# Kernel tuning notes

Measured on AMD Instinct MI355X. Metric: run time of the kernel, lower is better.

Reference implementation:

```python
import jax, jax.numpy as jnp
import numpy as np

N_NODES = 50000
N_EDGES = 800000
D_FEAT = 128
UNITS = 256
K = 3


def setup_inputs() -> dict:
    key = jax.random.key(0)
    k1, k2, k3, k4 = jax.random.split(key, 4)
    x = jax.random.normal(k1, (N_NODES, D_FEAT), dtype=jnp.float32)
    edge_index = jax.random.randint(k2, (2, N_EDGES), 0, N_NODES, dtype=jnp.int32)
    edge_weight = jnp.ones((N_EDGES,), dtype=jnp.float32)
    # glorot-uniform kernel [(K+1)*D, UNITS], zero bias
    fan_in, fan_out = D_FEAT * (K + 1), UNITS
    limit = np.sqrt(6.0 / (fan_in + fan_out)).astype(np.float32)
    kernel = jax.random.uniform(k3, (fan_in, fan_out), minval=-limit, maxval=limit, dtype=jnp.float32)
    bias = jnp.zeros((UNITS,), dtype=jnp.float32)
    return {"x": x, "edge_index": edge_index, "edge_weight": edge_weight,
            "kernel": kernel, "bias": bias}


def reference(x, edge_index, edge_weight, kernel, bias):
    n = x.shape[0]
    row, col = edge_index[0], edge_index[1]
    # symmetric GCN normalization (renorm=False: normalize first, then self-loops w=1)
    deg = jax.ops.segment_sum(edge_weight, row, num_segments=n)
    deg_inv_sqrt = jnp.where(deg > 0, jax.lax.rsqrt(jnp.where(deg > 0, deg, 1.0)), 0.0)
    normed_w = deg_inv_sqrt[row] * edge_weight * deg_inv_sqrt[col]
    loop = jnp.arange(n, dtype=row.dtype)
    row2 = jnp.concatenate([row, loop])
    col2 = jnp.concatenate([col, loop])
    w2 = jnp.concatenate([normed_w, jnp.ones((n,), dtype=normed_w.dtype)])
    # K-hop propagation, collecting each hop
    xs = [x]
    h = x
    for _ in range(K):
        msg = h[col2] * w2[:, None]            # [E+N, D] gather + scale
        h = jax.ops.segment_sum(msg, row2, num_segments=n)  # scatter-sum
        xs.append(h)
    hcat = jnp.concatenate(xs, axis=-1)        # [N, (K+1)*D]
    out = hcat @ kernel + bias
    return jax.nn.relu(out)
```

## Files before the change

### kernel.cpp

```cpp
#include <hip/hip_runtime.h>

#define NN 50000
#define NP 50048
#define NE 800000
#define D 128
#define UNITS 256
#define KTOT 512
#define SCAN_NB 50
#define NREP 16
#define CONV_NB 6250

typedef __attribute__((ext_vector_type(8))) short short8;
typedef __attribute__((ext_vector_type(4))) float floatx4;

__device__ inline unsigned short f2b(float f) {
    unsigned u = __float_as_uint(f);
    return (unsigned short)((u + 0x7fff + ((u >> 16) & 1)) >> 16);
}
__device__ inline float2 bx2f(unsigned v) {
    float2 r;
    r.x = __uint_as_float(v << 16);
    r.y = __uint_as_float(v & 0xffff0000u);
    return r;
}

__global__ void count_kernel(const int* __restrict__ row, int* __restrict__ cnt16,
                             int* __restrict__ rank, int E) {
    int e = blockIdx.x * blockDim.x + threadIdx.x;
    if (e < E) {
        int rep = (e >> 6) & (NREP - 1);
        rank[e] = atomicAdd(&cnt16[rep * NN + row[e]], 1);
    }
}

__global__ __launch_bounds__(256) void scanA_kernel(int* __restrict__ cnt16,
                                                    int* __restrict__ row_ptr,
                                                    int* __restrict__ bsum) {
    __shared__ int s[256];
    int b = blockIdx.x, t = threadIdx.x;
    int base = b * 1024 + t * 4;
    int v[4];
    int sum = 0;
#pragma unroll
    for (int i = 0; i < 4; ++i) {
        int idx = base + i;
        int tot = 0;
        if (idx < NN) {
            int c[NREP];
            int run = 0;
#pragma unroll
            for (int r = 0; r < NREP; ++r) c[r] = cnt16[r * NN + idx];
#pragma unroll
            for (int r = 0; r < NREP; ++r) {
                cnt16[r * NN + idx] = run;
                run += c[r];
            }
            tot = run;
        }
        v[i] = tot;
        sum += tot;
    }
    s[t] = sum;
    __syncthreads();
    for (int off = 1; off < 256; off <<= 1) {
        int add = (t >= off) ? s[t - off] : 0;
        __syncthreads();
        s[t] += add;
        __syncthreads();
    }
    int run = s[t] - sum;
#pragma unroll
    for (int i = 0; i < 4; ++i) {
        int idx = base + i;
        if (idx < NN) row_ptr[idx] = run;
        run += v[i];
    }
    if (t == 255) bsum[b] = s[255];
}

__global__ void scanB_kernel(int* __restrict__ bsum, int* __restrict__ row_ptr) {
    if (threadIdx.x == 0 && blockIdx.x == 0) {
        int run = 0;
        for (int i = 0; i < SCAN_NB; ++i) {
            int v = bsum[i];
            bsum[i] = run;
            run += v;
        }
        row_ptr[NN] = run;
    }
}

__global__ __launch_bounds__(256) void scanC_kernel(int* __restrict__ row_ptr,
                                                    const int* __restrict__ bsum) {
    int b = blockIdx.x, t = threadIdx.x;
    int off = bsum[b];
    int base = b * 1024 + t * 4;
#pragma unroll
    for (int i = 0; i < 4; ++i) {
        int idx = base + i;
        if (idx < NN) row_ptr[idx] += off;
    }
}

__global__ void fill_kernel(const int* __restrict__ row, const int* __restrict__ col,
                            const float* __restrict__ w, const int* __restrict__ rank,
                            const int* __restrict__ row_ptr, const int* __restrict__ cnt16,
                            int2* __restrict__ edges, int E) {
    int e = blockIdx.x * blockDim.x + threadIdx.x;
    if (e >= E) return;
    int r = row[e];
    int rep = (e >> 6) & (NREP - 1);
    int pos = row_ptr[r] + cnt16[rep * NN + r] + rank[e];
    edges[pos] = make_int2(col[e], __float_as_int(w[e]));
}

__global__ __launch_bounds__(256) void degdis_kernel(const int* __restrict__ row_ptr,
                                                     const int2* __restrict__ edges,
                                                     float* __restrict__ dis) {
    int node = blockIdx.x * 4 + (threadIdx.x >> 6);
    int l = threadIdx.x & 63;
    if (node >= NN) return;
    int beg = row_ptr[node], end = row_ptr[node + 1];
    float s = 0.f;
    for (int e = beg + l; e < end; e += 64) s += __int_as_float(edges[e].y);
#pragma unroll
    for (int off = 32; off; off >>= 1) s += __shfl_down(s, off);
    if (l == 0) dis[node] = s > 0.f ? rsqrtf(s) : 0.f;
}

__global__ __launch_bounds__(256) void prep_kernel(const float* __restrict__ x,
                                                   unsigned* __restrict__ xb,
                                                   const float* __restrict__ W,
                                                   short* __restrict__ Wt) {
    __shared__ float tile[32][33];
    if (blockIdx.x < CONV_NB) {
        int t = blockIdx.x * 256 + threadIdx.x;
        float4 v = ((const float4*)x)[t];
        uint2 o;
        o.x = (unsigned)f2b(v.x) | ((unsigned)f2b(v.y) << 16);
        o.y = (unsigned)f2b(v.z) | ((unsigned)f2b(v.w) << 16);
        ((uint2*)xb)[t] = o;
    } else {
        int b = blockIdx.x - CONV_NB;
        int kb = (b & 15) * 32;
        int nb = (b >> 4) * 32;
        int tx = threadIdx.x & 31, ty = threadIdx.x >> 5;
        for (int i = 0; i < 32; i += 8)
            tile[ty + i][tx] = W[(size_t)(kb + ty + i) * UNITS + nb + tx];
        __syncthreads();
        for (int i = 0; i < 32; i += 8)
            Wt[(size_t)(nb + ty + i) * KTOT + kb + tx] = (short)f2b(tile[tx][ty + i]);
    }
}

__device__ inline void acc8(float* acc, uint4 v, float w) {
    float2 f0 = bx2f(v.x), f1 = bx2f(v.y), f2 = bx2f(v.z), f3 = bx2f(v.w);
    acc[0] = fmaf(w, f0.x, acc[0]); acc[1] = fmaf(w, f0.y, acc[1]);
    acc[2] = fmaf(w, f1.x, acc[2]); acc[3] = fmaf(w, f1.y, acc[3]);
    acc[4] = fmaf(w, f2.x, acc[4]); acc[5] = fmaf(w, f2.y, acc[5]);
    acc[6] = fmaf(w, f3.x, acc[6]); acc[7] = fmaf(w, f3.y, acc[7]);
}

template <bool NORM>
__global__ __launch_bounds__(256) void gather_kernel(const unsigned* __restrict__ hprev,
                                                     unsigned* __restrict__ hnext,
                                                     const int* __restrict__ row_ptr,
                                                     int2* __restrict__ edges,
                                                     const float* __restrict__ dis) {
    int node = blockIdx.x * 4 + (threadIdx.x >> 6);
    if (node >= NN) return;
    int l = threadIdx.x & 63;
    int g = l >> 4;
    int s = l & 15;
    const uint4* hp4 = (const uint4*)hprev;
    int beg = row_ptr[node], end = row_ptr[node + 1];
    float dr = NORM ? dis[node] : 1.f;

    float acc[8] = {0.f, 0.f, 0.f, 0.f, 0.f, 0.f, 0.f, 0.f};
    int2 M0 = edges[(beg + g) < end ? (beg + g) : end - 1];
    int2 M1 = edges[(beg + 4 + g) < end ? (beg + 4 + g) : end - 1];
    for (int e = beg; e < end; e += 8) {
        int i0 = e + g;
        int i1 = e + 4 + g;
        int2 E0 = M0, E1 = M1;
        int en = e + 8;
        if (en < end) {
            int j0 = en + g, j1 = en + 4 + g;
            M0 = edges[j0 < end ? j0 : end - 1];
            M1 = edges[j1 < end ? j1 : end - 1];
        }
        float w0 = __int_as_float(E0.y);
        float w1 = __int_as_float(E1.y);
        if (NORM) {
            w0 *= dr * dis[E0.x];
            w1 *= dr * dis[E1.x];
        }
        w0 = (i0 < end) ? w0 : 0.f;
        w1 = (i1 < end) ? w1 : 0.f;
        uint4 v0 = hp4[(size_t)E0.x * 16 + s];
        uint4 v1 = hp4[(size_t)E1.x * 16 + s];
        acc8(acc, v0, w0);
        acc8(acc, v1, w1);
        if (NORM && s == 0) {
            if (i0 < end) edges[i0].y = __float_as_int(w0);
            if (i1 < end) edges[i1].y = __float_as_int(w1);
        }
    }
#pragma unroll
    for (int i = 0; i < 8; ++i) {
        acc[i] += __shfl_xor(acc[i], 16);
        acc[i] += __shfl_xor(acc[i], 32);
    }
    if (g == 0) {
        uint4 sv = hp4[(size_t)node * 16 + s];
        acc8(acc, sv, 1.f);
        uint4 o;
        o.x = (unsigned)f2b(acc[0]) | ((unsigned)f2b(acc[1]) << 16);
        o.y = (unsigned)f2b(acc[2]) | ((unsigned)f2b(acc[3]) << 16);
        o.z = (unsigned)f2b(acc[4]) | ((unsigned)f2b(acc[5]) << 16);
        o.w = (unsigned)f2b(acc[6]) | ((unsigned)f2b(acc[7]) << 16);
        ((uint4*)hnext)[(size_t)node * 16 + s] = o;
    }
}

#define BK 64
#define GLDS(g, l)                                                                      \
    __builtin_amdgcn_global_load_lds((const __attribute__((address_space(1))) void*)(g), \
                                     (__attribute__((address_space(3))) void*)(l), 16, 0, 0)

__global__ __launch_bounds__(256) void gemm_mfma(const short* __restrict__ A0,
                                                 const short* __restrict__ Wt,
                                                 const float* __restrict__ bias,
                                                 float* __restrict__ C) {
    __shared__ short As[128 * BK];
    __shared__ short Bs[128 * BK];
    const int t = threadIdx.x;
    const int m0 = blockIdx.x * 128;
    const int n0 = blockIdx.y * 128;
    const int w = t >> 6;
    const int l = t & 63;
    const int wr = (w >> 1) * 64;
    const int wc = (w & 1) * 64;
    const int lm = l & 15;
    const int lg = l >> 4;

    const int srow = l >> 3;
    const int soff = ((l & 7) ^ srow) * 8;

    floatx4 zero = {0.f, 0.f, 0.f, 0.f};
    floatx4 acc[4][4];
#pragma unroll
    for (int r = 0; r < 4; ++r)
#pragma unroll
        for (int c = 0; c < 4; ++c) acc[r][c] = zero;

    for (int kk = 0; kk < KTOT; kk += BK) {
        const short* Asrc = A0 + (size_t)(kk >> 7) * ((size_t)NP * 128) + (kk & 127);
        const short* Bsrc = Wt + kk;
#pragma unroll
        for (int i = 0; i < 4; ++i) {
            int seg = w * 4 + i;
            int row = seg * 8 + srow;
            GLDS(Asrc + (size_t)(m0 + row) * D + soff, As + seg * 512);
            GLDS(Bsrc + (size_t)(n0 + row) * KTOT + soff, Bs + seg * 512);
        }
        __syncthreads();
#pragma unroll
        for (int j = 0; j < 2; ++j) {
            short8 af[4], bfr[4];
#pragma unroll
            for (int r = 0; r < 4; ++r) {
                int row = wr + r * 16 + lm;
                int ch = (lg + 4 * j) ^ (row & 7);
                af[r] = *(const short8*)&As[row * BK + ch * 8];
            }
#pragma unroll
            for (int c = 0; c < 4; ++c) {
                int row = wc + c * 16 + lm;
                int ch = (lg + 4 * j) ^ (row & 7);
                bfr[c] = *(const short8*)&Bs[row * BK + ch * 8];
            }
#pragma unroll
            for (int r = 0; r < 4; ++r)
#pragma unroll
                for (int c = 0; c < 4; ++c)
                    acc[r][c] = __builtin_amdgcn_mfma_f32_16x16x32_bf16(af[r], bfr[c],
                                                                        acc[r][c], 0, 0, 0);
        }
        __syncthreads();
    }

    const int q4 = lg * 4;
#pragma unroll
    for (int r = 0; r < 4; ++r) {
#pragma unroll
        for (int i = 0; i < 4; ++i) {
            int m = m0 + wr + r * 16 + q4 + i;
            if (m < NN) {
#pragma unroll
                for (int c = 0; c < 4; ++c) {
                    int n = n0 + wc + c * 16 + lm;
                    float v = acc[r][c][i] + bias[n];
                    C[(size_t)m * UNITS + n] = fmaxf(v, 0.f);
                }
            }
        }
    }
}

extern "C" void kernel_launch(void* const* d_in, const int* in_sizes, int n_in,
                              void* d_out, int out_size, void* d_ws, size_t ws_size,
                              hipStream_t stream) {
    const float* x = (const float*)d_in[0];
    const int* ei = (const int*)d_in[1];
    const float* ew_in = (const float*)d_in[2];
    const float* W = (const float*)d_in[3];
    const float* bias = (const float*)d_in[4];
    float* out = (float*)d_out;

    const int* row = ei;
    const int* col = ei + NE;

    float* dis = (float*)d_ws;
    int* cnt16 = (int*)(dis + NN);
    int* rank = cnt16 + NREP * NN;
    int* bsum = rank + NE;
    int* row_ptr = bsum + 64;
    int2* edges = (int2*)(row_ptr + NN + 2);
    unsigned* xb = (unsigned*)(edges + NE) + 2;
    unsigned* h1b = xb + (size_t)NP * 64;
    unsigned* h2b = h1b + (size_t)NP * 64;
    unsigned* h3b = h2b + (size_t)NP * 64;
    short* Wt = (short*)(h3b + (size_t)NP * 64);

    hipMemsetAsync(cnt16, 0, NREP * NN * sizeof(int), stream);

    count_kernel<<<(NE + 255) / 256, 256, 0, stream>>>(row, cnt16, rank, NE);
    scanA_kernel<<<SCAN_NB, 256, 0, stream>>>(cnt16, row_ptr, bsum);
    scanB_kernel<<<1, 64, 0, stream>>>(bsum, row_ptr);
    scanC_kernel<<<SCAN_NB, 256, 0, stream>>>(row_ptr, bsum);
    fill_kernel<<<(NE + 255) / 256, 256, 0, stream>>>(row, col, ew_in, rank, row_ptr, cnt16,
                                                      edges, NE);
    degdis_kernel<<<(NN + 3) / 4, 256, 0, stream>>>(row_ptr, edges, dis);
    prep_kernel<<<CONV_NB + 128, 256, 0, stream>>>(x, xb, W, Wt);

    int gat_blocks = (NN + 3) / 4;
    gather_kernel<true><<<gat_blocks, 256, 0, stream>>>(xb, h1b, row_ptr, edges, dis);
    gather_kernel<false><<<gat_blocks, 256, 0, stream>>>(h1b, h2b, row_ptr, edges, dis);
    gather_kernel<false><<<gat_blocks, 256, 0, stream>>>(h2b, h3b, row_ptr, edges, dis);

    gemm_mfma<<<dim3(NP / 128, UNITS / 128), 256, 0, stream>>>(
        (const short*)xb, Wt, bias, out);
}
```

Baseline: 315.3 us.

## Fuse preprocessing kernels, compute degree by atomics, widen gather, double-buffer GEMM

The count, x/W conversion and degree computation now run in one launch, with degree accumulated by float atomics instead of a separate CSR-walking kernel. The scan drops its single-thread middle kernel and instead has each block reduce the preceding block sums. The gather loop handles 16 edges per iteration with four outstanding row loads, up from 8. The GEMM moves to 64x128 tiles with BK=32 and double-buffered LDS staging. Together these cut launch count and improve overlap, at the cost of atomic contention on the degree array and more GEMM iterations.

```diff
diff --git a/kernel.cpp b/kernel.cpp
--- a/kernel.cpp
+++ b/kernel.cpp
@@ -6,9 +6,10 @@
 #define D 128
 #define UNITS 256
 #define KTOT 512
-#define SCAN_NB 50
+#define SCAN_NB 196
 #define NREP 16
 #define CONV_NB 6250
+#define COUNT_NB 3125
 
 typedef __attribute__((ext_vector_type(8))) short short8;
 typedef __attribute__((ext_vector_type(4))) float floatx4;
@@ -24,43 +25,69 @@
     return r;
 }
 
-__global__ void count_kernel(const int* __restrict__ row, int* __restrict__ cnt16,
-                             int* __restrict__ rank, int E) {
-    int e = blockIdx.x * blockDim.x + threadIdx.x;
-    if (e < E) {
-        int rep = (e >> 6) & (NREP - 1);
-        rank[e] = atomicAdd(&cnt16[rep * NN + row[e]], 1);
+__global__ __launch_bounds__(256) void count_prep_kernel(const int* __restrict__ row,
+                                                         const float* __restrict__ ew,
+                                                         int* __restrict__ cnt16,
+                                                         float* __restrict__ deg,
+                                                         int* __restrict__ rank,
+                                                         const float* __restrict__ x,
+                                                         unsigned* __restrict__ xb,
+                                                         const float* __restrict__ W,
+                                                         short* __restrict__ Wt) {
+    __shared__ float tile[32][33];
+    int b = blockIdx.x;
+    if (b < COUNT_NB) {
+        int e = b * 256 + threadIdx.x;
+        if (e < NE) {
+            int r = row[e];
+            int rep = (e >> 6) & (NREP - 1);
+            rank[e] = atomicAdd(&cnt16[rep * NN + r], 1);
+            atomicAdd(&deg[r], ew[e]);
+        }
+    } else if (b < COUNT_NB + CONV_NB) {
+        int t = (b - COUNT_NB) * 256 + threadIdx.x;
+        float4 v = ((const float4*)x)[t];
+        uint2 o;
+        o.x = (unsigned)f2b(v.x) | ((unsigned)f2b(v.y) << 16);
+        o.y = (unsigned)f2b(v.z) | ((unsigned)f2b(v.w) << 16);
+        ((uint2*)xb)[t] = o;
+    } else {
+        int bb = b - COUNT_NB - CONV_NB;
+        int kb = (bb & 15) * 32;
+        int nb = (bb >> 4) * 32;
+        int tx = threadIdx.x & 31, ty = threadIdx.x >> 5;
+        for (int i = 0; i < 32; i += 8)
+            tile[ty + i][tx] = W[(size_t)(kb + ty + i) * UNITS + nb + tx];
+        __syncthreads();
+        for (int i = 0; i < 32; i += 8)
+            Wt[(size_t)(nb + ty + i) * KTOT + kb + tx] = (short)f2b(tile[tx][ty + i]);
     }
 }
 
 __global__ __launch_bounds__(256) void scanA_kernel(int* __restrict__ cnt16,
+                                                    const float* __restrict__ deg,
+                                                    float* __restrict__ dis,
                                                     int* __restrict__ row_ptr,
                                                     int* __restrict__ bsum) {
     __shared__ int s[256];
-    int b = blockIdx.x, t = threadIdx.x;
-    int base = b * 1024 + t * 4;
-    int v[4];
-    int sum = 0;
-#pragma unroll
-    for (int i = 0; i < 4; ++i) {
-        int idx = base + i;
-        int tot = 0;
-        if (idx < NN) {
-            int c[NREP];
-            int run = 0;
-#pragma unroll
-            for (int r = 0; r < NREP; ++r) c[r] = cnt16[r * NN + idx];
-#pragma unroll
-            for (int r = 0; r < NREP; ++r) {
-                cnt16[r * NN + idx] = run;
-                run += c[r];
-            }
-            tot = run;
-        }
-        v[i] = tot;
-        sum += tot;
-    }
-    s[t] = sum;
+    int t = threadIdx.x;
+    int idx = blockIdx.x * 256 + t;
+    int tot = 0;
+    if (idx < NN) {
+        int c[NREP];
+#pragma unroll
+        for (int r = 0; r < NREP; ++r) c[r] = cnt16[r * NN + idx];
+        int run = 0;
+#pragma unroll
+        for (int r = 0; r < NREP; ++r) {
+            cnt16[r * NN + idx] = run;
+            run += c[r];
+        }
+        tot = run;
+        float dv = deg[idx];
+        dis[idx] = dv > 0.f ? rsqrtf(dv) : 0.f;
+    }
+    s[t] = tot;
     __syncthreads();
     for (int off = 1; off < 256; off <<= 1) {
         int add = (t >= off) ? s[t - off] : 0;
@@ -68,38 +95,25 @@
         s[t] += add;
         __syncthreads();
     }
-    int run = s[t] - sum;
-#pragma unroll
-    for (int i = 0; i < 4; ++i) {
-        int idx = base + i;
-        if (idx < NN) row_ptr[idx] = run;
-        run += v[i];
-    }
-    if (t == 255) bsum[b] = s[255];
-}
-
-__global__ void scanB_kernel(int* __restrict__ bsum, int* __restrict__ row_ptr) {
-    if (threadIdx.x == 0 && blockIdx.x == 0) {
-        int run = 0;
-        for (int i = 0; i < SCAN_NB; ++i) {
-            int v = bsum[i];
-            bsum[i] = run;
-            run += v;
-        }
-        row_ptr[NN] = run;
-    }
+    if (idx < NN) row_ptr[idx] = s[t] - tot;
+    if (t == 255) bsum[blockIdx.x] = s[255];
 }
 
 __global__ __launch_bounds__(256) void scanC_kernel(int* __restrict__ row_ptr,
                                                     const int* __restrict__ bsum) {
+    __shared__ int soff_s;
     int b = blockIdx.x, t = threadIdx.x;
-    int off = bsum[b];
-    int base = b * 1024 + t * 4;
-#pragma unroll
-    for (int i = 0; i < 4; ++i) {
-        int idx = base + i;
-        if (idx < NN) row_ptr[idx] += off;
-    }
+    if (t < 64) {
+        int acc = 0;
+        for (int i = t; i < b; i += 64) acc += bsum[i];
+#pragma unroll
+        for (int off = 32; off; off >>= 1) acc += __shfl_down(acc, off);
+        if (t == 0) soff_s = acc;
+    }
+    __syncthreads();
+    int idx = b * 256 + t;
+    if (idx < NN) row_ptr[idx] += soff_s;
+    if (b == 0 && t == 0) row_ptr[NN] = NE;
 }
 
 __global__ void fill_kernel(const int* __restrict__ row, const int* __restrict__ col,
@@ -112,45 +126,6 @@
     int rep = (e >> 6) & (NREP - 1);
     int pos = row_ptr[r] + cnt16[rep * NN + r] + rank[e];
     edges[pos] = make_int2(col[e], __float_as_int(w[e]));
-}
-
-__global__ __launch_bounds__(256) void degdis_kernel(const int* __restrict__ row_ptr,
-                                                     const int2* __restrict__ edges,
-                                                     float* __restrict__ dis) {
-    int node = blockIdx.x * 4 + (threadIdx.x >> 6);
-    int l = threadIdx.x & 63;
-    if (node >= NN) return;
-    int beg = row_ptr[node], end = row_ptr[node + 1];
-    float s = 0.f;
-    for (int e = beg + l; e < end; e += 64) s += __int_as_float(edges[e].y);
-#pragma unroll
-    for (int off = 32; off; off >>= 1) s += __shfl_down(s, off);
-    if (l == 0) dis[node] = s > 0.f ? rsqrtf(s) : 0.f;
-}
-
-__global__ __launch_bounds__(256) void prep_kernel(const float* __restrict__ x,
-                                                   unsigned* __restrict__ xb,
-                                                   const float* __restrict__ W,
-                                                   short* __restrict__ Wt) {
-    __shared__ float tile[32][33];
-    if (blockIdx.x < CONV_NB) {
-        int t = blockIdx.x * 256 + threadIdx.x;
-        float4 v = ((const float4*)x)[t];
-        uint2 o;
-        o.x = (unsigned)f2b(v.x) | ((unsigned)f2b(v.y) << 16);
-        o.y = (unsigned)f2b(v.z) | ((unsigned)f2b(v.w) << 16);
-        ((uint2*)xb)[t] = o;
-    } else {
-        int b = blockIdx.x - CONV_NB;
-        int kb = (b & 15) * 32;
-        int nb = (b >> 4) * 32;
-        int tx = threadIdx.x & 31, ty = threadIdx.x >> 5;
-        for (int i = 0; i < 32; i += 8)
-            tile[ty + i][tx] = W[(size_t)(kb + ty + i) * UNITS + nb + tx];
-        __syncthreads();
-        for (int i = 0; i < 32; i += 8)
-            Wt[(size_t)(nb + ty + i) * KTOT + kb + tx] = (short)f2b(tile[tx][ty + i]);
-    }
 }
 
 __device__ inline void acc8(float* acc, uint4 v, float w) {
@@ -175,35 +150,46 @@
     const uint4* hp4 = (const uint4*)hprev;
     int beg = row_ptr[node], end = row_ptr[node + 1];
     float dr = NORM ? dis[node] : 1.f;
+    int last = (end - 1 > beg) ? end - 1 : beg;
+    if (last >= NE) last = NE - 1;
 
     float acc[8] = {0.f, 0.f, 0.f, 0.f, 0.f, 0.f, 0.f, 0.f};
-    int2 M0 = edges[(beg + g) < end ? (beg + g) : end - 1];
-    int2 M1 = edges[(beg + 4 + g) < end ? (beg + 4 + g) : end - 1];
-    for (int e = beg; e < end; e += 8) {
-        int i0 = e + g;
-        int i1 = e + 4 + g;
-        int2 E0 = M0, E1 = M1;
-        int en = e + 8;
+    int2 M[4];
+#pragma unroll
+    for (int b = 0; b < 4; ++b) {
+        int i = beg + b * 4 + g;
+        M[b] = edges[i < end ? i : last];
+    }
+    for (int e = beg; e < end; e += 16) {
+        int2 E[4];
+#pragma unroll
+        for (int b = 0; b < 4; ++b) E[b] = M[b];
+        int en = e + 16;
         if (en < end) {
-            int j0 = en + g, j1 = en + 4 + g;
-            M0 = edges[j0 < end ? j0 : end - 1];
-            M1 = edges[j1 < end ? j1 : end - 1];
-        }
-        float w0 = __int_as_float(E0.y);
-        float w1 = __int_as_float(E1.y);
-        if (NORM) {
-            w0 *= dr * dis[E0.x];
-            w1 *= dr * dis[E1.x];
-        }
-        w0 = (i0 < end) ? w0 : 0.f;
-        w1 = (i1 < end) ? w1 : 0.f;
-        uint4 v0 = hp4[(size_t)E0.x * 16 + s];
-        uint4 v1 = hp4[(size_t)E1.x * 16 + s];
-        acc8(acc, v0, w0);
-        acc8(acc, v1, w1);
+#pragma unroll
+            for (int b = 0; b < 4; ++b) {
+                int j = en + b * 4 + g;
+                M[b] = edges[j < end ? j : last];
+            }
+        }
+        float wgt[4];
+        uint4 v[4];
+#pragma unroll
+        for (int b = 0; b < 4; ++b) {
+            float wv = __int_as_float(E[b].y);
+            if (NORM) wv *= dr * dis[E[b].x];
+            int i = e + b * 4 + g;
+            wgt[b] = (i < end) ? wv : 0.f;
+            v[b] = hp4[(size_t)E[b].x * 16 + s];
+        }
+#pragma unroll
+        for (int b = 0; b < 4; ++b) acc8(acc, v[b], wgt[b]);
         if (NORM && s == 0) {
-            if (i0 < end) edges[i0].y = __float_as_int(w0);
-            if (i1 < end) edges[i1].y = __float_as_int(w1);
+#pragma unroll
+            for (int b = 0; b < 4; ++b) {
+                int i = e + b * 4 + g;
+                if (i < end) edges[i].y = __float_as_int(wgt[b]);
+            }
         }
     }
 #pragma unroll
@@ -223,7 +209,8 @@
     }
 }
 
-#define BK 64
+#define BK 32
+#define NIT (KTOT / BK)
 #define GLDS(g, l)                                                                      \
     __builtin_amdgcn_global_load_lds((const __attribute__((address_space(1))) void*)(g), \
                                      (__attribute__((address_space(3))) void*)(l), 16, 0, 0)
@@ -232,67 +219,70 @@
                                                  const short* __restrict__ Wt,
                                                  const float* __restrict__ bias,
                                                  float* __restrict__ C) {
-    __shared__ short As[128 * BK];
-    __shared__ short Bs[128 * BK];
+    __shared__ short As[2][64 * BK];
+    __shared__ short Bs[2][128 * BK];
     const int t = threadIdx.x;
-    const int m0 = blockIdx.x * 128;
+    const int m0 = blockIdx.x * 64;
     const int n0 = blockIdx.y * 128;
     const int w = t >> 6;
     const int l = t & 63;
-    const int wr = (w >> 1) * 64;
+    const int wr = (w >> 1) * 32;
     const int wc = (w & 1) * 64;
     const int lm = l & 15;
     const int lg = l >> 4;
-
-    const int srow = l >> 3;
-    const int soff = ((l & 7) ^ srow) * 8;
+    const int srow = l >> 2;
+    const int soff = ((l & 3) ^ ((l >> 3) & 3)) * 8;
 
     floatx4 zero = {0.f, 0.f, 0.f, 0.f};
-    floatx4 acc[4][4];
-#pragma unroll
-    for (int r = 0; r < 4; ++r)
+    floatx4 acc[2][4];
+#pragma unroll
+    for (int r = 0; r < 2; ++r)
 #pragma unroll
         for (int c = 0; c < 4; ++c) acc[r][c] = zero;
 
-    for (int kk = 0; kk < KTOT; kk += BK) {
-        const short* Asrc = A0 + (size_t)(kk >> 7) * ((size_t)NP * 128) + (kk & 127);
-        const short* Bsrc = Wt + kk;
-#pragma unroll
-        for (int i = 0; i < 4; ++i) {
-            int seg = w * 4 + i;
-            int row = seg * 8 + srow;
-            GLDS(Asrc + (size_t)(m0 + row) * D + soff, As + seg * 512);
-            GLDS(Bsrc + (size_t)(n0 + row) * KTOT + soff, Bs + seg * 512);
-        }
+#define STAGE(IT, BUF)                                                                  \
+    do {                                                                                \
+        int kk = (IT) * BK;                                                             \
+        const short* Asrc = A0 + (size_t)(kk >> 7) * ((size_t)NP * 128) + (kk & 127);   \
+        const short* Bsrc = Wt + kk;                                                    \
+        GLDS(Asrc + (size_t)(m0 + w * 16 + srow) * D + soff, &As[BUF][w * 512]);        \
+        GLDS(Bsrc + (size_t)(n0 + (2 * w) * 16 + srow) * KTOT + soff,                   \
+             &Bs[BUF][(2 * w) * 512]);                                                  \
+        GLDS(Bsrc + (size_t)(n0 + (2 * w + 1) * 16 + srow) * KTOT + soff,               \
+             &Bs[BUF][(2 * w + 1) * 512]);                                              \
+    } while (0)
+
+    STAGE(0, 0);
+    __syncthreads();
+    for (int it = 0; it < NIT; ++it) {
+        int cur = it & 1;
+        if (it + 1 < NIT) STAGE(it + 1, cur ^ 1);
+        short8 af[2], bf[4];
+#pragma unroll
+        for (int r = 0; r < 2; ++r) {
+            int rowv = wr + r * 16 + lm;
+            int p = lg ^ ((rowv >> 1) & 3);
+            af[r] = *(const short8*)&As[cur][rowv * BK + p * 8];
+        }
+#pragma unroll
+        for (int c = 0; c < 4; ++c) {
+            int rowv = wc + c * 16 + lm;
+            int p = lg ^ ((rowv >> 1) & 3);
+            bf[c] = *(const short8*)&Bs[cur][rowv * BK + p * 8];
+        }
+#pragma unroll
+        for (int r = 0; r < 2; ++r)
+#pragma unroll
+            for (int c = 0; c < 4; ++c)
+                acc[r][c] = __builtin_amdgcn_mfma_f32_16x16x32_bf16(af[r], bf[c],
+                                                                    acc[r][c], 0, 0, 0);
         __syncthreads();
-#pragma unroll
-        for (int j = 0; j < 2; ++j) {
-            short8 af[4], bfr[4];
-#pragma unroll
-            for (int r = 0; r < 4; ++r) {
-                int row = wr + r * 16 + lm;
-                int ch = (lg + 4 * j) ^ (row & 7);
-                af[r] = *(const short8*)&As[row * BK + ch * 8];
-            }
-#pragma unroll
-            for (int c = 0; c < 4; ++c) {
-                int row = wc + c * 16 + lm;
-                int ch = (lg + 4 * j) ^ (row & 7);
-                bfr[c] = *(const short8*)&Bs[row * BK + ch * 8];
-            }
-#pragma unroll
-            for (int r = 0; r < 4; ++r)
-#pragma unroll
-                for (int c = 0; c < 4; ++c)
-                    acc[r][c] = __builtin_amdgcn_mfma_f32_16x16x32_bf16(af[r], bfr[c],
-                                                                        acc[r][c], 0, 0, 0);
-        }
-        __syncthreads();
-    }
+    }
+#undef STAGE
 
     const int q4 = lg * 4;
 #pragma unroll
-    for (int r = 0; r < 4; ++r) {
+    for (int r = 0; r < 2; ++r) {
 #pragma unroll
         for (int i = 0; i < 4; ++i) {
             int m = m0 + wr + r * 16 + q4 + i;
@@ -323,32 +313,31 @@
 
     float* dis = (float*)d_ws;
     int* cnt16 = (int*)(dis + NN);
-    int* rank = cnt16 + NREP * NN;
+    float* deg = (float*)(cnt16 + NREP * NN);
+    int* rank = (int*)(deg + NN);
     int* bsum = rank + NE;
-    int* row_ptr = bsum + 64;
+    int* row_ptr = bsum + 256;
     int2* edges = (int2*)(row_ptr + NN + 2);
-    unsigned* xb = (unsigned*)(edges + NE) + 2;
+    unsigned* xb = (unsigned*)(((uintptr_t)(edges + NE) + 15) & ~(uintptr_t)15);
     unsigned* h1b = xb + (size_t)NP * 64;
     unsigned* h2b = h1b + (size_t)NP * 64;
     unsigned* h3b = h2b + (size_t)NP * 64;
     short* Wt = (short*)(h3b + (size_t)NP * 64);
 
-    hipMemsetAsync(cnt16, 0, NREP * NN * sizeof(int), stream);
-
-    count_kernel<<<(NE + 255) / 256, 256, 0, stream>>>(row, cnt16, rank, NE);
-    scanA_kernel<<<SCAN_NB, 256, 0, stream>>>(cnt16, row_ptr, bsum);
-    scanB_kernel<<<1, 64, 0, stream>>>(bsum, row_ptr);
+    hipMemsetAsync(cnt16, 0, (NREP * NN + NN) * sizeof(int), stream);
+
+    count_prep_kernel<<<COUNT_NB + CONV_NB + 128, 256, 0, stream>>>(row, ew_in, cnt16, deg,
+                                                                    rank, x, xb, W, Wt);
+    scanA_kernel<<<SCAN_NB, 256, 0, stream>>>(cnt16, deg, dis, row_ptr, bsum);
     scanC_kernel<<<SCAN_NB, 256, 0, stream>>>(row_ptr, bsum);
     fill_kernel<<<(NE + 255) / 256, 256, 0, stream>>>(row, col, ew_in, rank, row_ptr, cnt16,
                                                       edges, NE);
-    degdis_kernel<<<(NN + 3) / 4, 256, 0, stream>>>(row_ptr, edges, dis);
-    prep_kernel<<<CONV_NB + 128, 256, 0, stream>>>(x, xb, W, Wt);
 
     int gat_blocks = (NN + 3) / 4;
     gather_kernel<true><<<gat_blocks, 256, 0, stream>>>(xb, h1b, row_ptr, edges, dis);
     gather_kernel<false><<<gat_blocks, 256, 0, stream>>>(h1b, h2b, row_ptr, edges, dis);
     gather_kernel<false><<<gat_blocks, 256, 0, stream>>>(h2b, h3b, row_ptr, edges, dis);
 
-    gemm_mfma<<<dim3(NP / 128, UNITS / 128), 256, 0, stream>>>(
+    gemm_mfma<<<dim3(NP / 64, UNITS / 128), 256, 0, stream>>>(
         (const short*)xb, Wt, bias, out);
 }
```

Measured after the change: 343.1 us. 1.09x slower.
